# Optimization experiments

Measured on AMD Instinct MI355X. Metric: run time of the kernel, lower is better.

The kernel has to match this reference:

```python
import jax, jax.numpy as jnp
import numpy as np

TOP_K = 2


def setup_inputs() -> dict:
    key = jax.random.key(0)
    k1, k2 = jax.random.split(key)
    x = jax.random.normal(k1, (16384, 2048), dtype=jnp.float32)
    gate_w = jax.random.normal(k2, (2048, 64), dtype=jnp.float32) * (1.0 / np.sqrt(2048))
    gate_b = jnp.zeros((64,), dtype=jnp.float32)
    return {"x": x, "gate_w": gate_w, "gate_b": gate_b}


def reference(x, gate_w, gate_b):
    num_tokens = x.shape[0]
    num_experts = gate_w.shape[1]
    # gate linear: [N, d_model] @ [d_model, E] -> [N, E]
    gate_logits = x @ gate_w + gate_b
    # top-k selection and renormalized softmax over selected logits
    top_k_logits, selected_experts = jax.lax.top_k(gate_logits, TOP_K)
    top_k_weights = jax.nn.softmax(top_k_logits, axis=-1)
    rows = jnp.arange(num_tokens)[:, None]  # [N, 1]
    gate_weights = jnp.zeros_like(gate_logits).at[rows, selected_experts].set(top_k_weights)
    # auxiliary load-balancing loss
    expert_mask = jnp.zeros_like(gate_logits).at[rows, selected_experts].set(1.0)
    tokens_per_expert = expert_mask.sum(axis=0)  # [E]
    fraction_per_expert = tokens_per_expert / (num_tokens * TOP_K)
    mean_prob_per_expert = jax.nn.softmax(gate_logits, axis=-1).mean(axis=0)  # [E]
    aux_loss = num_experts * jnp.sum(fraction_per_expert * mean_prob_per_expert)
    return gate_weights, selected_experts, aux_loss
```

## Files before the change

kernel.cpp:

```cpp
#include <hip/hip_runtime.h>
#include <math.h>

#define NTOK 16384
#define KDIM 2048
#define NEXP 64
#define NWAVE 16
#define BLOCK (NWAVE * 64)
#define KS (KDIM / NWAVE)
#define XC 8
#define NXC (KS / XC)
#define RPAD 68

typedef float f4 __attribute__((ext_vector_type(4)));
typedef float f16v __attribute__((ext_vector_type(16)));

__global__ __launch_bounds__(BLOCK, 4) void gate_main(
    const float* __restrict__ x, const float* __restrict__ gw,
    const float* __restrict__ gb, float* __restrict__ out_w,
    float* __restrict__ out_idx, float* __restrict__ ws)
{
    __shared__ float red[2 * 64 * RPAD];
    __shared__ float meta[64 * 4];
    __shared__ float scnt[NEXP];

    const int tid  = threadIdx.x;
    const int lane = tid & 63;
    const int wid  = __builtin_amdgcn_readfirstlane(tid >> 6);
    const int row  = blockIdx.x * 64 + lane;

    const float* xrow  = x  + (size_t)row * KDIM + wid * KS;
    const float* wbase = gw + (size_t)wid * KS * NEXP;

    float acc[NEXP];
#pragma unroll
    for (int e = 0; e < NEXP; ++e) acc[e] = 0.f;

    f4 xa = *(const f4*)(xrow);
    f4 xb = *(const f4*)(xrow + 4);
    for (int c = 0; c < NXC; ++c) {
        const int cn = (c + 1 < NXC) ? (c + 1) : c;
        f4 na = *(const f4*)(xrow + cn * XC);
        f4 nb = *(const f4*)(xrow + cn * XC + 4);
        const float xs[XC] = {xa.x, xa.y, xa.z, xa.w, xb.x, xb.y, xb.z, xb.w};
#pragma unroll
        for (int j = 0; j < XC; ++j) {
            const f16v* wr = (const f16v*)(wbase + (size_t)(c * XC + j) * NEXP);
#pragma unroll
            for (int q = 0; q < 4; ++q) {
                const f16v wv = wr[q];
#pragma unroll
                for (int t = 0; t < 16; ++t)
                    acc[q * 16 + t] = fmaf(xs[j], wv[t], acc[q * 16 + t]);
            }
        }
        xa = na; xb = nb;
    }

    for (int half = NWAVE / 2; half >= 1; half >>= 1) {
        for (int sub = 0; sub < half; sub += 2) {
            const int nslot = (half - sub < 2) ? (half - sub) : 2;
            __syncthreads();
            if (wid >= half + sub && wid < half + sub + nslot) {
                float* dst = red + (size_t)(wid - half - sub) * 64 * RPAD + lane * RPAD;
#pragma unroll
                for (int q = 0; q < 16; ++q) {
                    f4 v = {acc[q*4+0], acc[q*4+1], acc[q*4+2], acc[q*4+3]};
                    *(f4*)(dst + q * 4) = v;
                }
            }
            __syncthreads();
            if (wid >= sub && wid < sub + nslot) {
                const float* src = red + (size_t)(wid - sub) * 64 * RPAD + lane * RPAD;
#pragma unroll
                for (int q = 0; q < 16; ++q) {
                    f4 v = *(const f4*)(src + q * 4);
                    acc[q*4+0] += v.x; acc[q*4+1] += v.y;
                    acc[q*4+2] += v.z; acc[q*4+3] += v.w;
                }
            }
        }
    }

    __syncthreads();
    int i1 = 0, i2 = 0;
    if (wid == 0) {
#pragma unroll
        for (int e = 0; e < NEXP; ++e) acc[e] += gb[e];

        float v1 = acc[0];
#pragma unroll
        for (int e = 1; e < NEXP; ++e)
            if (acc[e] > v1) { v1 = acc[e]; i1 = e; }
        float v2 = -INFINITY;
#pragma unroll
        for (int e = 0; e < NEXP; ++e)
            if (e != i1 && acc[e] > v2) { v2 = acc[e]; i2 = e; }

        float ssum = 0.f;
#pragma unroll
        for (int e = 0; e < NEXP; ++e) ssum += __expf(acc[e] - v1);
        const float sinv = 1.f / ssum;
        float* pr = red + (size_t)lane * RPAD;
#pragma unroll
        for (int e = 0; e < NEXP; ++e) pr[e] = __expf(acc[e] - v1) * sinv;

        const float e2 = __expf(v2 - v1);
        const float w1 = 1.f / (1.f + e2);
        f4 m = {(float)i1, (float)i2, w1, e2 * w1};
        ((f4*)meta)[lane] = m;

        float2 idx2 = make_float2((float)i1, (float)i2);
        *(float2*)(out_idx + (size_t)row * 2) = idx2;

        scnt[lane] = 0.f;
        atomicAdd(&scnt[i1], 1.f);
        atomicAdd(&scnt[i2], 1.f);
    }
    __syncthreads();
    if (wid == 0) {
        float ps = 0.f;
#pragma unroll
        for (int r = 0; r < 64; ++r) ps += red[(size_t)r * RPAD + lane];
        atomicAdd(&ws[lane], ps);
        atomicAdd(&ws[NEXP + lane], scnt[lane]);
    }
    __syncthreads();

#pragma unroll
    for (int rr = 0; rr < 4; ++rr) {
        const int r = wid * 4 + rr;
        const f4 m = ((const f4*)meta)[r];
        const float val = (lane == (int)m.x) ? m.z
                        : ((lane == (int)m.y) ? m.w : 0.f);
        out_w[((size_t)blockIdx.x * 64 + r) * NEXP + lane] = val;
    }
}

__global__ void gate_aux(const float* __restrict__ ws, float* __restrict__ out_aux)
{
    const int e = threadIdx.x;
    const float frac = ws[NEXP + e] * (1.f / (float)(NTOK * 2));
    const float mp   = ws[e] * (1.f / (float)NTOK);
    float v = frac * mp * (float)NEXP;
#pragma unroll
    for (int off = 32; off; off >>= 1) v += __shfl_xor(v, off);
    if (e == 0) out_aux[0] = v;
}

extern "C" void kernel_launch(void* const* d_in, const int* in_sizes, int n_in,
                              void* d_out, int out_size, void* d_ws, size_t ws_size,
                              hipStream_t stream) {
    const float* x  = (const float*)d_in[0];
    const float* gw = (const float*)d_in[1];
    const float* gb = (const float*)d_in[2];

    float* out     = (float*)d_out;
    float* out_w   = out;
    float* out_idx = out + (size_t)NTOK * NEXP;
    float* out_aux = out_idx + (size_t)NTOK * 2;
    float* ws      = (float*)d_ws;

    hipMemsetAsync(ws, 0, 2 * NEXP * sizeof(float), stream);
    gate_main<<<NTOK / 64, BLOCK, 0, stream>>>(x, gw, gb, out_w, out_idx, ws);
    gate_aux<<<1, 64, 0, stream>>>(ws, out_aux);
}
```

Before: 91.59 us.

## Register-tile gate GEMM as 4 rows x 16 experts per lane with packed FMA

Changes the per-lane work split of the gate matmul. Each lane previously computed all 64 experts for one row, reading weights as wave-uniform values. Now each lane computes a 4-row by 16-expert tile, using packed 2-wide FMAs, with per-lane vector weight loads and four x rows prefetched. Lanes now load distinct weight columns and x data is shared across rows in registers, which may raise arithmetic intensity and allow v_pk_fma. The cost is an extra shared-memory transpose so that wave 0 can regather full rows for top-k and softmax.

```diff
diff --git a/kernel.cpp b/kernel.cpp
--- a/kernel.cpp
+++ b/kernel.cpp
@@ -4,15 +4,13 @@
 #define NTOK 16384
 #define KDIM 2048
 #define NEXP 64
-#define NWAVE 16
-#define BLOCK (NWAVE * 64)
-#define KS (KDIM / NWAVE)
-#define XC 8
-#define NXC (KS / XC)
+#define NW   16
+#define BLOCK (NW * 64)
+#define KS   (KDIM / NW)
 #define RPAD 68
 
+typedef float f2 __attribute__((ext_vector_type(2)));
 typedef float f4 __attribute__((ext_vector_type(4)));
-typedef float f16v __attribute__((ext_vector_type(16)));
 
 __global__ __launch_bounds__(BLOCK, 4) void gate_main(
     const float* __restrict__ x, const float* __restrict__ gw,
@@ -23,40 +21,67 @@
     __shared__ float meta[64 * 4];
     __shared__ float scnt[NEXP];
 
-    const int tid  = threadIdx.x;
-    const int lane = tid & 63;
-    const int wid  = __builtin_amdgcn_readfirstlane(tid >> 6);
-    const int row  = blockIdx.x * 64 + lane;
-
-    const float* xrow  = x  + (size_t)row * KDIM + wid * KS;
-    const float* wbase = gw + (size_t)wid * KS * NEXP;
-
-    float acc[NEXP];
-#pragma unroll
-    for (int e = 0; e < NEXP; ++e) acc[e] = 0.f;
-
-    f4 xa = *(const f4*)(xrow);
-    f4 xb = *(const f4*)(xrow + 4);
-    for (int c = 0; c < NXC; ++c) {
-        const int cn = (c + 1 < NXC) ? (c + 1) : c;
-        f4 na = *(const f4*)(xrow + cn * XC);
-        f4 nb = *(const f4*)(xrow + cn * XC + 4);
-        const float xs[XC] = {xa.x, xa.y, xa.z, xa.w, xb.x, xb.y, xb.z, xb.w};
-#pragma unroll
-        for (int j = 0; j < XC; ++j) {
-            const f16v* wr = (const f16v*)(wbase + (size_t)(c * XC + j) * NEXP);
-#pragma unroll
-            for (int q = 0; q < 4; ++q) {
-                const f16v wv = wr[q];
-#pragma unroll
-                for (int t = 0; t < 16; ++t)
-                    acc[q * 16 + t] = fmaf(xs[j], wv[t], acc[q * 16 + t]);
+    const int tid   = threadIdx.x;
+    const int lane  = tid & 63;
+    const int wid   = __builtin_amdgcn_readfirstlane(tid >> 6);
+    const int es    = lane & 3;
+    const int rs    = lane >> 2;
+    const int e0    = es * 16;
+    const int rbase = blockIdx.x * 64;
+    const int k0    = wid * KS;
+
+    const float* xbase = x + (size_t)(rbase + rs * 4) * KDIM + k0;
+    const float* wrow0 = gw + (size_t)k0 * NEXP + e0;
+
+    f2 a[4][8];
+#pragma unroll
+    for (int i = 0; i < 4; ++i)
+#pragma unroll
+        for (int p = 0; p < 8; ++p) a[i][p] = (f2){0.f, 0.f};
+
+    f4 w0 = *(const f4*)(wrow0 + 0);
+    f4 w1 = *(const f4*)(wrow0 + 4);
+    f4 w2 = *(const f4*)(wrow0 + 8);
+    f4 w3 = *(const f4*)(wrow0 + 12);
+    f4 x0 = *(const f4*)(xbase + 0 * (size_t)KDIM);
+    f4 x1 = *(const f4*)(xbase + 1 * (size_t)KDIM);
+    f4 x2 = *(const f4*)(xbase + 2 * (size_t)KDIM);
+    f4 x3 = *(const f4*)(xbase + 3 * (size_t)KDIM);
+
+    for (int c = 0; c < KS / 4; ++c) {
+        const int cn = (c + 1 < KS / 4) ? c + 1 : c;
+        f4 nx0 = *(const f4*)(xbase + 0 * (size_t)KDIM + cn * 4);
+        f4 nx1 = *(const f4*)(xbase + 1 * (size_t)KDIM + cn * 4);
+        f4 nx2 = *(const f4*)(xbase + 2 * (size_t)KDIM + cn * 4);
+        f4 nx3 = *(const f4*)(xbase + 3 * (size_t)KDIM + cn * 4);
+#pragma unroll
+        for (int j = 0; j < 4; ++j) {
+            const int k  = c * 4 + j;
+            const int kn = (k + 1 < KS) ? k + 1 : k;
+            const f2 xs0 = {x0[j], x0[j]};
+            const f2 xs1 = {x1[j], x1[j]};
+            const f2 xs2 = {x2[j], x2[j]};
+            const f2 xs3 = {x3[j], x3[j]};
+#pragma unroll
+            for (int p = 0; p < 8; ++p) {
+                const f4 cc = (p >> 1) == 0 ? w0 : (p >> 1) == 1 ? w1
+                            : (p >> 1) == 2 ? w2 : w3;
+                const f2 wl = {cc[2 * (p & 1)], cc[2 * (p & 1) + 1]};
+                a[0][p] = __builtin_elementwise_fma(xs0, wl, a[0][p]);
+                a[1][p] = __builtin_elementwise_fma(xs1, wl, a[1][p]);
+                a[2][p] = __builtin_elementwise_fma(xs2, wl, a[2][p]);
+                a[3][p] = __builtin_elementwise_fma(xs3, wl, a[3][p]);
             }
+            const float* wn = gw + (size_t)(k0 + kn) * NEXP + e0;
+            w0 = *(const f4*)(wn + 0);
+            w1 = *(const f4*)(wn + 4);
+            w2 = *(const f4*)(wn + 8);
+            w3 = *(const f4*)(wn + 12);
         }
-        xa = na; xb = nb;
-    }
-
-    for (int half = NWAVE / 2; half >= 1; half >>= 1) {
+        x0 = nx0; x1 = nx1; x2 = nx2; x3 = nx3;
+    }
+
+    for (int half = NW / 2; half >= 1; half >>= 1) {
         for (int sub = 0; sub < half; sub += 2) {
             const int nslot = (half - sub < 2) ? (half - sub) : 2;
             __syncthreads();
@@ -64,7 +89,8 @@
                 float* dst = red + (size_t)(wid - half - sub) * 64 * RPAD + lane * RPAD;
 #pragma unroll
                 for (int q = 0; q < 16; ++q) {
-                    f4 v = {acc[q*4+0], acc[q*4+1], acc[q*4+2], acc[q*4+3]};
+                    f4 v = {a[q >> 2][(q & 3) * 2].x,     a[q >> 2][(q & 3) * 2].y,
+                            a[q >> 2][(q & 3) * 2 + 1].x, a[q >> 2][(q & 3) * 2 + 1].y};
                     *(f4*)(dst + q * 4) = v;
                 }
             }
@@ -74,43 +100,61 @@
 #pragma unroll
                 for (int q = 0; q < 16; ++q) {
                     f4 v = *(const f4*)(src + q * 4);
-                    acc[q*4+0] += v.x; acc[q*4+1] += v.y;
-                    acc[q*4+2] += v.z; acc[q*4+3] += v.w;
+                    a[q >> 2][(q & 3) * 2].x     += v.x;
+                    a[q >> 2][(q & 3) * 2].y     += v.y;
+                    a[q >> 2][(q & 3) * 2 + 1].x += v.z;
+                    a[q >> 2][(q & 3) * 2 + 1].y += v.w;
                 }
             }
         }
     }
 
     __syncthreads();
+    if (wid == 0) {
+#pragma unroll
+        for (int i = 0; i < 4; ++i)
+#pragma unroll
+            for (int p = 0; p < 8; ++p)
+                *(f2*)(red + (size_t)(rs * 4 + i) * RPAD + e0 + 2 * p) = a[i][p];
+    }
+    __syncthreads();
+
     int i1 = 0, i2 = 0;
     if (wid == 0) {
-#pragma unroll
-        for (int e = 0; e < NEXP; ++e) acc[e] += gb[e];
-
-        float v1 = acc[0];
+        float lg[64];
+#pragma unroll
+        for (int q = 0; q < 16; ++q) {
+            f4 v = *(const f4*)(red + (size_t)lane * RPAD + q * 4);
+            lg[q * 4 + 0] = v.x; lg[q * 4 + 1] = v.y;
+            lg[q * 4 + 2] = v.z; lg[q * 4 + 3] = v.w;
+        }
+#pragma unroll
+        for (int e = 0; e < NEXP; ++e) lg[e] += gb[e];
+
+        float v1 = lg[0];
 #pragma unroll
         for (int e = 1; e < NEXP; ++e)
-            if (acc[e] > v1) { v1 = acc[e]; i1 = e; }
+            if (lg[e] > v1) { v1 = lg[e]; i1 = e; }
         float v2 = -INFINITY;
 #pragma unroll
         for (int e = 0; e < NEXP; ++e)
-            if (e != i1 && acc[e] > v2) { v2 = acc[e]; i2 = e; }
+            if (e != i1 && lg[e] > v2) { v2 = lg[e]; i2 = e; }
 
         float ssum = 0.f;
 #pragma unroll
-        for (int e = 0; e < NEXP; ++e) ssum += __expf(acc[e] - v1);
+        for (int e = 0; e < NEXP; ++e) ssum += __expf(lg[e] - v1);
         const float sinv = 1.f / ssum;
         float* pr = red + (size_t)lane * RPAD;
 #pragma unroll
-        for (int e = 0; e < NEXP; ++e) pr[e] = __expf(acc[e] - v1) * sinv;
+        for (int e = 0; e < NEXP; ++e) pr[e] = __expf(lg[e] - v1) * sinv;
 
         const float e2 = __expf(v2 - v1);
-        const float w1 = 1.f / (1.f + e2);
-        f4 m = {(float)i1, (float)i2, w1, e2 * w1};
+        const float wa = 1.f / (1.f + e2);
+        f4 m = {(float)i1, (float)i2, wa, e2 * wa};
         ((f4*)meta)[lane] = m;
 
-        float2 idx2 = make_float2((float)i1, (float)i2);
-        *(float2*)(out_idx + (size_t)row * 2) = idx2;
+        *(float2*)(out_idx + (size_t)(rbase + lane) * 2) =
+            make_float2((float)i1, (float)i2);
 
         scnt[lane] = 0.f;
         atomicAdd(&scnt[i1], 1.f);
@@ -132,7 +176,7 @@
         const f4 m = ((const f4*)meta)[r];
         const float val = (lane == (int)m.x) ? m.z
                         : ((lane == (int)m.y) ? m.w : 0.f);
-        out_w[((size_t)blockIdx.x * 64 + r) * NEXP + lane] = val;
+        out_w[((size_t)rbase + r) * NEXP + lane] = val;
     }
 }
 
@@ -160,7 +204,7 @@
     float* out_aux = out_idx + (size_t)NTOK * 2;
     float* ws      = (float*)d_ws;
 
-    hipMemsetAsync(ws, 0, 2 * NEXP * sizeof(float), stream);
+    (void)hipMemsetAsync(ws, 0, 2 * NEXP * sizeof(float), stream);
     gate_main<<<NTOK / 64, BLOCK, 0, stream>>>(x, gw, gb, out_w, out_idx, ws);
     gate_aux<<<1, 64, 0, stream>>>(ws, out_aux);
 }
```

After: 220.2 us. 2.4x slower.

## Split K across two blocks with partial logits and separate top-k finish kernel

Applied to the files above, without the earlier changes.

The GEMM is split into two K halves handled by separate blocks, doubling the grid, and each block writes partial logits to workspace. A new finish kernel sums the partials, adds the bias and computes top-2, softmax, per-expert counts and probability sums using wave shuffles. Weight rows are loaded with inline-asm scalar loads (s_load_dwordx16) in both the split and monolithic kernels, and the monolithic kernel remains as a fallback when the workspace is too small. The split is meant to raise parallelism and spread the per-row epilogue across waves, at the cost of an extra kernel launch and a round trip of partial logits through global memory.

```diff
diff --git a/kernel.cpp b/kernel.cpp
--- a/kernel.cpp
+++ b/kernel.cpp
@@ -4,32 +4,43 @@
 #define NTOK 16384
 #define KDIM 2048
 #define NEXP 64
-#define NWAVE 16
-#define BLOCK (NWAVE * 64)
-#define KS (KDIM / NWAVE)
-#define XC 8
-#define NXC (KS / XC)
+#define NW   16
+#define BLOCK (NW * 64)
 #define RPAD 68
+#define PSZ  ((size_t)NTOK * NEXP)
 
 typedef float f4 __attribute__((ext_vector_type(4)));
-typedef float f16v __attribute__((ext_vector_type(16)));
-
-__global__ __launch_bounds__(BLOCK, 4) void gate_main(
+typedef float f16s __attribute__((ext_vector_type(16)));
+
+#define LOAD_W_ROW(wA, wB, wC, wD, wk)                                  \
+    do {                                                                \
+        asm volatile("s_load_dwordx16 %0, %4, 0x0\n\t"                  \
+                     "s_load_dwordx16 %1, %4, 0x40\n\t"                 \
+                     "s_load_dwordx16 %2, %4, 0x80\n\t"                 \
+                     "s_load_dwordx16 %3, %4, 0xc0"                     \
+                     : "=&s"(wA), "=&s"(wB), "=&s"(wC), "=&s"(wD)       \
+                     : "s"(wk));                                        \
+        asm volatile("s_waitcnt lgkmcnt(0)"                             \
+                     : "+s"(wA), "+s"(wB), "+s"(wC), "+s"(wD));         \
+    } while (0)
+
+__global__ __launch_bounds__(BLOCK, 4) void gate_gemm(
     const float* __restrict__ x, const float* __restrict__ gw,
-    const float* __restrict__ gb, float* __restrict__ out_w,
-    float* __restrict__ out_idx, float* __restrict__ ws)
+    float* __restrict__ p0, float* __restrict__ p1)
 {
     __shared__ float red[2 * 64 * RPAD];
-    __shared__ float meta[64 * 4];
-    __shared__ float scnt[NEXP];
 
     const int tid  = threadIdx.x;
     const int lane = tid & 63;
     const int wid  = __builtin_amdgcn_readfirstlane(tid >> 6);
-    const int row  = blockIdx.x * 64 + lane;
-
-    const float* xrow  = x  + (size_t)row * KDIM + wid * KS;
-    const float* wbase = gw + (size_t)wid * KS * NEXP;
+    const int rg   = blockIdx.x >> 1;
+    const int kq   = blockIdx.x & 1;
+    const int row  = rg * 64 + lane;
+    const int KS   = 64;
+    const int k0   = kq * (KDIM / 2) + wid * KS;
+
+    const float* xrow  = x  + (size_t)row * KDIM + k0;
+    const float* wbase = gw + (size_t)k0 * NEXP;
 
     float acc[NEXP];
 #pragma unroll
@@ -37,26 +48,30 @@
 
     f4 xa = *(const f4*)(xrow);
     f4 xb = *(const f4*)(xrow + 4);
-    for (int c = 0; c < NXC; ++c) {
-        const int cn = (c + 1 < NXC) ? (c + 1) : c;
-        f4 na = *(const f4*)(xrow + cn * XC);
-        f4 nb = *(const f4*)(xrow + cn * XC + 4);
-        const float xs[XC] = {xa.x, xa.y, xa.z, xa.w, xb.x, xb.y, xb.z, xb.w};
-#pragma unroll
-        for (int j = 0; j < XC; ++j) {
-            const f16v* wr = (const f16v*)(wbase + (size_t)(c * XC + j) * NEXP);
-#pragma unroll
-            for (int q = 0; q < 4; ++q) {
-                const f16v wv = wr[q];
-#pragma unroll
-                for (int t = 0; t < 16; ++t)
-                    acc[q * 16 + t] = fmaf(xs[j], wv[t], acc[q * 16 + t]);
-            }
+    for (int c = 0; c < KS / 8; ++c) {
+        const int cn = (c + 1 < KS / 8) ? (c + 1) : c;
+        f4 na = *(const f4*)(xrow + cn * 8);
+        f4 nb = *(const f4*)(xrow + cn * 8 + 4);
+        const float xs[8] = {xa[0], xa[1], xa[2], xa[3],
+                             xb[0], xb[1], xb[2], xb[3]};
+#pragma unroll
+        for (int j = 0; j < 8; ++j) {
+            const float* wk = wbase + (size_t)(c * 8 + j) * NEXP;
+            f16s wA, wB, wC, wD;
+            LOAD_W_ROW(wA, wB, wC, wD, wk);
+#pragma unroll
+            for (int t = 0; t < 16; ++t) acc[t]      = fmaf(xs[j], wA[t], acc[t]);
+#pragma unroll
+            for (int t = 0; t < 16; ++t) acc[16 + t] = fmaf(xs[j], wB[t], acc[16 + t]);
+#pragma unroll
+            for (int t = 0; t < 16; ++t) acc[32 + t] = fmaf(xs[j], wC[t], acc[32 + t]);
+#pragma unroll
+            for (int t = 0; t < 16; ++t) acc[48 + t] = fmaf(xs[j], wD[t], acc[48 + t]);
         }
         xa = na; xb = nb;
     }
 
-    for (int half = NWAVE / 2; half >= 1; half >>= 1) {
+    for (int half = NW / 2; half >= 1; half >>= 1) {
         for (int sub = 0; sub < half; sub += 2) {
             const int nslot = (half - sub < 2) ? (half - sub) : 2;
             __syncthreads();
@@ -82,11 +97,165 @@
     }
 
     __syncthreads();
+    if (wid == 0) {
+#pragma unroll
+        for (int q = 0; q < 16; ++q) {
+            f4 v = {acc[q*4+0], acc[q*4+1], acc[q*4+2], acc[q*4+3]};
+            *(f4*)(red + (size_t)lane * RPAD + q * 4) = v;
+        }
+    }
+    __syncthreads();
+    float* dst = (kq == 0 ? p0 : p1) + (size_t)rg * 64 * NEXP;
+    ((f4*)dst)[tid] = *(const f4*)(red + (size_t)(tid >> 4) * RPAD + (tid & 15) * 4);
+}
+
+#define W2 16
+__global__ __launch_bounds__(1024) void gate_finish(
+    const float* __restrict__ p0, const float* __restrict__ p1,
+    const float* __restrict__ gb, float* __restrict__ out_w,
+    float* __restrict__ out_idx, float* __restrict__ aux)
+{
+    __shared__ float red[2 * W2 * NEXP];
+    const int tid  = threadIdx.x;
+    const int lane = tid & 63;
+    const int wid  = tid >> 6;
+
+    float psum = 0.f, cnt = 0.f;
+#pragma unroll
+    for (int rr = 0; rr < 4; ++rr) {
+        const size_t row = (size_t)blockIdx.x * 64 + wid * 4 + rr;
+        const size_t o   = row * NEXP + lane;
+        const float l = p0[o] + p1[o] + gb[lane];
+
+        float v1 = l; int i1 = lane;
+#pragma unroll
+        for (int off = 32; off; off >>= 1) {
+            const float ov = __shfl_xor(v1, off);
+            const int   oi = __shfl_xor(i1, off);
+            if (ov > v1 || (ov == v1 && oi < i1)) { v1 = ov; i1 = oi; }
+        }
+        float v2 = (lane == i1) ? -INFINITY : l; int i2 = lane;
+#pragma unroll
+        for (int off = 32; off; off >>= 1) {
+            const float ov = __shfl_xor(v2, off);
+            const int   oi = __shfl_xor(i2, off);
+            if (ov > v2 || (ov == v2 && oi < i2)) { v2 = ov; i2 = oi; }
+        }
+
+        const float p = __expf(l - v1);
+        float s = p;
+#pragma unroll
+        for (int off = 32; off; off >>= 1) s += __shfl_xor(s, off);
+        psum += p / s;
+        cnt  += ((lane == i1) ? 1.f : 0.f) + ((lane == i2) ? 1.f : 0.f);
+
+        const float e2 = __expf(v2 - v1);
+        const float wa = 1.f / (1.f + e2);
+        out_w[o] = (lane == i1) ? wa : ((lane == i2) ? e2 * wa : 0.f);
+        if (lane == 0)
+            *(float2*)(out_idx + row * 2) = make_float2((float)i1, (float)i2);
+    }
+
+    red[wid * NEXP + lane]             = psum;
+    red[W2 * NEXP + wid * NEXP + lane] = cnt;
+    __syncthreads();
+    if (tid < 2 * NEXP) {
+        const int half = tid >> 6, e = tid & 63;
+        float v = 0.f;
+#pragma unroll
+        for (int w = 0; w < W2; ++w) v += red[half * W2 * NEXP + w * NEXP + e];
+        atomicAdd(&aux[half * NEXP + e], v);
+    }
+}
+
+__global__ void gate_aux(const float* __restrict__ aux, float* __restrict__ out_aux)
+{
+    const int e = threadIdx.x;
+    const float frac = aux[NEXP + e] * (1.f / (float)(NTOK * 2));
+    const float mp   = aux[e] * (1.f / (float)NTOK);
+    float v = frac * mp * (float)NEXP;
+#pragma unroll
+    for (int off = 32; off; off >>= 1) v += __shfl_xor(v, off);
+    if (e == 0) out_aux[0] = v;
+}
+
+#define MKS (KDIM / NW)
+__global__ __launch_bounds__(BLOCK, 4) void gate_mono(
+    const float* __restrict__ x, const float* __restrict__ gw,
+    const float* __restrict__ gb, float* __restrict__ out_w,
+    float* __restrict__ out_idx, float* __restrict__ ws)
+{
+    __shared__ float red[2 * 64 * RPAD];
+    __shared__ float meta[64 * 4];
+    __shared__ float scnt[NEXP];
+
+    const int tid  = threadIdx.x;
+    const int lane = tid & 63;
+    const int wid  = __builtin_amdgcn_readfirstlane(tid >> 6);
+    const int row  = blockIdx.x * 64 + lane;
+
+    const float* xrow  = x  + (size_t)row * KDIM + wid * MKS;
+    const float* wbase = gw + (size_t)wid * MKS * NEXP;
+
+    float acc[NEXP];
+#pragma unroll
+    for (int e = 0; e < NEXP; ++e) acc[e] = 0.f;
+
+    f4 xa = *(const f4*)(xrow);
+    f4 xb = *(const f4*)(xrow + 4);
+    for (int c = 0; c < MKS / 8; ++c) {
+        const int cn = (c + 1 < MKS / 8) ? (c + 1) : c;
+        f4 na = *(const f4*)(xrow + cn * 8);
+        f4 nb = *(const f4*)(xrow + cn * 8 + 4);
+        const float xs[8] = {xa[0], xa[1], xa[2], xa[3],
+                             xb[0], xb[1], xb[2], xb[3]};
+#pragma unroll
+        for (int j = 0; j < 8; ++j) {
+            const float* wk = wbase + (size_t)(c * 8 + j) * NEXP;
+            f16s wA, wB, wC, wD;
+            LOAD_W_ROW(wA, wB, wC, wD, wk);
+#pragma unroll
+            for (int t = 0; t < 16; ++t) acc[t]      = fmaf(xs[j], wA[t], acc[t]);
+#pragma unroll
+            for (int t = 0; t < 16; ++t) acc[16 + t] = fmaf(xs[j], wB[t], acc[16 + t]);
+#pragma unroll
+            for (int t = 0; t < 16; ++t) acc[32 + t] = fmaf(xs[j], wC[t], acc[32 + t]);
+#pragma unroll
+            for (int t = 0; t < 16; ++t) acc[48 + t] = fmaf(xs[j], wD[t], acc[48 + t]);
+        }
+        xa = na; xb = nb;
+    }
+
+    for (int half = NW / 2; half >= 1; half >>= 1) {
+        for (int sub = 0; sub < half; sub += 2) {
+            const int nslot = (half - sub < 2) ? (half - sub) : 2;
+            __syncthreads();
+            if (wid >= half + sub && wid < half + sub + nslot) {
+                float* dst = red + (size_t)(wid - half - sub) * 64 * RPAD + lane * RPAD;
+#pragma unroll
+                for (int q = 0; q < 16; ++q) {
+                    f4 v = {acc[q*4+0], acc[q*4+1], acc[q*4+2], acc[q*4+3]};
+                    *(f4*)(dst + q * 4) = v;
+                }
+            }
+            __syncthreads();
+            if (wid >= sub && wid < sub + nslot) {
+                const float* src = red + (size_t)(wid - sub) * 64 * RPAD + lane * RPAD;
+#pragma unroll
+                for (int q = 0; q < 16; ++q) {
+                    f4 v = *(const f4*)(src + q * 4);
+                    acc[q*4+0] += v.x; acc[q*4+1] += v.y;
+                    acc[q*4+2] += v.z; acc[q*4+3] += v.w;
+                }
+            }
+        }
+    }
+
+    __syncthreads();
     int i1 = 0, i2 = 0;
     if (wid == 0) {
 #pragma unroll
         for (int e = 0; e < NEXP; ++e) acc[e] += gb[e];
-
         float v1 = acc[0];
 #pragma unroll
         for (int e = 1; e < NEXP; ++e)
@@ -95,7 +264,6 @@
 #pragma unroll
         for (int e = 0; e < NEXP; ++e)
             if (e != i1 && acc[e] > v2) { v2 = acc[e]; i2 = e; }
-
         float ssum = 0.f;
 #pragma unroll
         for (int e = 0; e < NEXP; ++e) ssum += __expf(acc[e] - v1);
@@ -103,15 +271,11 @@
         float* pr = red + (size_t)lane * RPAD;
 #pragma unroll
         for (int e = 0; e < NEXP; ++e) pr[e] = __expf(acc[e] - v1) * sinv;
-
         const float e2 = __expf(v2 - v1);
         const float w1 = 1.f / (1.f + e2);
         f4 m = {(float)i1, (float)i2, w1, e2 * w1};
         ((f4*)meta)[lane] = m;
-
-        float2 idx2 = make_float2((float)i1, (float)i2);
-        *(float2*)(out_idx + (size_t)row * 2) = idx2;
-
+        *(float2*)(out_idx + (size_t)row * 2) = make_float2((float)i1, (float)i2);
         scnt[lane] = 0.f;
         atomicAdd(&scnt[i1], 1.f);
         atomicAdd(&scnt[i2], 1.f);
@@ -125,7 +289,6 @@
         atomicAdd(&ws[NEXP + lane], scnt[lane]);
     }
     __syncthreads();
-
 #pragma unroll
     for (int rr = 0; rr < 4; ++rr) {
         const int r = wid * 4 + rr;
@@ -136,17 +299,6 @@
     }
 }
 
-__global__ void gate_aux(const float* __restrict__ ws, float* __restrict__ out_aux)
-{
-    const int e = threadIdx.x;
-    const float frac = ws[NEXP + e] * (1.f / (float)(NTOK * 2));
-    const float mp   = ws[e] * (1.f / (float)NTOK);
-    float v = frac * mp * (float)NEXP;
-#pragma unroll
-    for (int off = 32; off; off >>= 1) v += __shfl_xor(v, off);
-    if (e == 0) out_aux[0] = v;
-}
-
 extern "C" void kernel_launch(void* const* d_in, const int* in_sizes, int n_in,
                               void* d_out, int out_size, void* d_ws, size_t ws_size,
                               hipStream_t stream) {
@@ -160,7 +312,18 @@
     float* out_aux = out_idx + (size_t)NTOK * 2;
     float* ws      = (float*)d_ws;
 
-    hipMemsetAsync(ws, 0, 2 * NEXP * sizeof(float), stream);
-    gate_main<<<NTOK / 64, BLOCK, 0, stream>>>(x, gw, gb, out_w, out_idx, ws);
-    gate_aux<<<1, 64, 0, stream>>>(ws, out_aux);
-}
+    const size_t need = (2 * PSZ + 2 * NEXP) * sizeof(float);
+    if (ws_size >= need) {
+        float* p0  = ws;
+        float* p1  = ws + PSZ;
+        float* aux = ws + 2 * PSZ;
+        (void)hipMemsetAsync(aux, 0, 2 * NEXP * sizeof(float), stream);
+        gate_gemm<<<(NTOK / 64) * 2, BLOCK, 0, stream>>>(x, gw, p0, p1);
+        gate_finish<<<NTOK / 64, 1024, 0, stream>>>(p0, p1, gb, out_w, out_idx, aux);
+        gate_aux<<<1, 64, 0, stream>>>(aux, out_aux);
+    } else {
+        (void)hipMemsetAsync(ws, 0, 2 * NEXP * sizeof(float), stream);
+        gate_mono<<<NTOK / 64, BLOCK, 0, stream>>>(x, gw, gb, out_w, out_idx, ws);
+        gate_aux<<<1, 64, 0, stream>>>(ws, out_aux);
+    }
+}
```

After: 124.3 us. +35.7%, slower.
